# Kernel optimization log

Measured on AMD Instinct MI355X. Metric: run time of the kernel, lower is better.

Reference implementation:

```python
import jax, jax.numpy as jnp
import numpy as np

SOS = 1  # letter2index['<sos>']
EOS = 0  # letter2index['<eos>'] (embedding padding_idx)

B, T, KV, E, H, V, L = 64, 2048, 128, 256, 512, 30, 256


def _lstm_cell(x, h, c, W_ih, W_hh, b_ih, b_hh):
    # PyTorch LSTMCell: gates ordered (i, f, g, o)
    gates = x @ W_ih.T + b_ih + h @ W_hh.T + b_hh
    i, f, g, o = jnp.split(gates, 4, axis=-1)
    c_new = jax.nn.sigmoid(f) * c + jax.nn.sigmoid(i) * jnp.tanh(g)
    h_new = jax.nn.sigmoid(o) * jnp.tanh(c_new)
    return h_new, c_new


def setup_inputs() -> dict:
    root = jax.random.key(0)
    ks = jax.random.split(root, 16)

    key = jax.random.normal(ks[0], (B, T, KV), dtype=jnp.float32)
    value = jax.random.normal(ks[1], (B, T, KV), dtype=jnp.float32)
    encoder_len = jax.random.randint(ks[2], (B,), 1, T + 1)
    y = jax.random.randint(ks[3], (B, L), 0, V)

    def w(k, shape, fan_in):
        return jax.random.normal(k, shape, dtype=jnp.float32) / np.sqrt(fan_in)

    emb_weight = w(ks[4], (V, E), E).at[EOS].set(0.0)  # padding_idx row zeroed
    in1 = E + KV
    W_ih1 = w(ks[5], (4 * H, in1), in1)
    W_hh1 = w(ks[6], (4 * H, H), H)
    b_ih1 = jnp.zeros((4 * H,), jnp.float32)
    b_hh1 = jnp.zeros((4 * H,), jnp.float32)
    W_ih2 = w(ks[7], (4 * KV, H), H)
    W_hh2 = w(ks[8], (4 * KV, KV), KV)
    b_ih2 = jnp.zeros((4 * KV,), jnp.float32)
    b_hh2 = jnp.zeros((4 * KV,), jnp.float32)
    out_bias = jnp.zeros((V,), jnp.float32)

    return dict(key=key, value=value, encoder_len=encoder_len, y=y,
                emb_weight=emb_weight,
                W_ih1=W_ih1, W_hh1=W_hh1, b_ih1=b_ih1, b_hh1=b_hh1,
                W_ih2=W_ih2, W_hh2=W_hh2, b_ih2=b_ih2, b_hh2=b_hh2,
                out_bias=out_bias)


def reference(key, value, encoder_len, y, emb_weight,
              W_ih1, W_hh1, b_ih1, b_hh1,
              W_ih2, W_hh2, b_ih2, b_hh2, out_bias):
    Bq, Tq, d_k = key.shape
    mask = jnp.arange(Tq)[None, :] >= encoder_len[:, None]  # (B, T) True = padded
    scale = 1.0 / np.sqrt(d_k).astype(np.float32)

    # Teacher forcing rate 1.0 in train mode: step i uses embed(SOS) at i=0,
    # embed(y[:, i-1]) afterwards.
    ids = jnp.concatenate([jnp.full((Bq, 1), SOS, dtype=y.dtype), y[:, :-1]], axis=1)
    embeds = emb_weight[ids]               # (B, L, E)
    embeds_t = jnp.swapaxes(embeds, 0, 1)  # (L, B, E)

    h_dim = W_hh1.shape[1]
    kv_dim = W_hh2.shape[1]
    init = (jnp.zeros((Bq, h_dim), key.dtype), jnp.zeros((Bq, h_dim), key.dtype),
            jnp.zeros((Bq, kv_dim), key.dtype), jnp.zeros((Bq, kv_dim), key.dtype),
            value.mean(axis=1))  # initial context

    def step(carry, char_embed):
        h1, c1, h2, c2, context = carry
        x = jnp.concatenate([char_embed, context], axis=1)
        h1, c1 = _lstm_cell(x, h1, c1, W_ih1, W_hh1, b_ih1, b_hh1)
        h2, c2 = _lstm_cell(h1, h2, c2, W_ih2, W_hh2, b_ih2, b_hh2)
        query = h2                                             # (B, KV)
        energy = jnp.einsum('bd,btd->bt', query, key) * scale  # (B, T)
        energy = jnp.where(mask, -1e9, energy)
        attn = jax.nn.softmax(energy, axis=1)
        ctx = jnp.einsum('bt,btd->bd', attn, value)            # (B, KV)
        logits = jnp.concatenate([query, ctx], axis=1) @ emb_weight.T + out_bias
        return (h1, c1, h2, c2, ctx), (logits, attn[0])

    _, (preds, attn_plot) = jax.lax.scan(step, init, embeds_t)
    predictions = jnp.swapaxes(preds, 0, 1)  # (B, L, V)
    return predictions, attn_plot            # attn_plot: (L, T), batch element 0
```

## Files before the change

kernel.cpp:

```cpp
#include <hip/hip_runtime.h>

#define NB 256
#define NT 1024

#define BB   64
#define TTS  2048
#define DKV  128
#define EEM  256
#define HH1  512
#define VVV  30
#define LLS  256
#define SOS_ID 1
#define SCALE_F 0.088388347648318447f

#define OFF_PM    0
#define OFF_PS    256
#define OFF_PCTX  512
#define OFF_WSE   33280
#define OFF_EMBT  35328
#define OFF_H1    68096
#define OFF_C1    133632
#define OFF_H2R   166400
#define OFF_H2T   182784
#define OFF_C2    199168
#define OFF_BAR   207360
#define OFF_KBF   212992
#define OFF_VBF   8601600
#define WS_NEED_BYTES 67960832ull
#define PRED_SZ   491520

struct Params {
  const float* key; const float* value;
  const int* enc_len; const int* y;
  const float* emb;
  const float* Wih1; const float* Whh1; const float* bih1; const float* bhh1;
  const float* Wih2; const float* Whh2; const float* bih2; const float* bhh2;
  const float* obias;
  float* out; float* ws;
};

struct SMEM {
  union {
    struct {
      float ctxT[8192];
      union { float wt[8192]; float red[8192]; } u;
    } a;
    struct { float wm[16]; float wS[16]; float wctx[2048]; } c;
  };
};

__device__ __forceinline__ float sigm(float x) { return 1.f / (1.f + __expf(-x)); }
__device__ __forceinline__ float tanh_f(float x) {
  float t = __expf(-2.f * fabsf(x));
  float r = (1.f - t) / (1.f + t);
  return x < 0.f ? -r : r;
}
__device__ __forceinline__ unsigned bfr(float f) {
  unsigned u = __float_as_uint(f);
  return (u + 0x7FFFu + ((u >> 16) & 1u)) >> 16;
}
__device__ __forceinline__ float b2f(unsigned short h) {
  return __uint_as_float(((unsigned)h) << 16);
}
__device__ __forceinline__ float blo(unsigned u) { return __uint_as_float(u << 16); }
__device__ __forceinline__ float bhi(unsigned u) { return __uint_as_float(u & 0xffff0000u); }

__device__ __forceinline__ void gbar(unsigned* base, unsigned expect) {
  __syncthreads();
  if (threadIdx.x == 0) {
    __builtin_amdgcn_fence(__ATOMIC_RELEASE, "agent");
    const int grp = blockIdx.x >> 3;
    unsigned* gcnt = base + grp * 32;
    if (__hip_atomic_fetch_add(gcnt, 1u, __ATOMIC_RELAXED, __HIP_MEMORY_SCOPE_AGENT) == 7u) {
      unsigned* mcnt = base + 1024;
      if (__hip_atomic_fetch_add(mcnt, 1u, __ATOMIC_RELAXED, __HIP_MEMORY_SCOPE_AGENT) == 31u) {
        __hip_atomic_store(mcnt, 0u, __ATOMIC_RELAXED, __HIP_MEMORY_SCOPE_AGENT);
        #pragma unroll
        for (int gg = 0; gg < 32; ++gg)
          __hip_atomic_store(base + gg * 32, 0u, __ATOMIC_RELAXED, __HIP_MEMORY_SCOPE_AGENT);
        __builtin_amdgcn_fence(__ATOMIC_RELEASE, "agent");
        #pragma unroll
        for (int gg = 0; gg < 32; ++gg)
          __hip_atomic_store(base + 2048 + gg * 32, expect, __ATOMIC_RELAXED, __HIP_MEMORY_SCOPE_AGENT);
      }
    }
    unsigned* mygen = base + 2048 + grp * 32;
    int guard = 0;
    while ((int)(__hip_atomic_load(mygen, __ATOMIC_RELAXED, __HIP_MEMORY_SCOPE_AGENT) - expect) < 0) {
      __builtin_amdgcn_s_sleep(8);
      if (++guard > 10000000) break;
    }
    __builtin_amdgcn_fence(__ATOMIC_ACQUIRE, "agent");
  }
  __syncthreads();
}

__device__ __forceinline__ void mac8x4(float acc[8][4], const float* wt, int k, float4 x4) {
  float4 wa = *(const float4*)(wt + k*8);
  float4 wb = *(const float4*)(wt + k*8 + 4);
  float wr[8] = {wa.x, wa.y, wa.z, wa.w, wb.x, wb.y, wb.z, wb.w};
  float xr[4] = {x4.x, x4.y, x4.z, x4.w};
  #pragma unroll
  for (int r = 0; r < 8; ++r)
    #pragma unroll
    for (int c = 0; c < 4; ++c)
      acc[r][c] += wr[r] * xr[c];
}

__device__ __forceinline__ void gate_reduce_store(float acc[8][4], float* red, int tid) {
  #pragma unroll
  for (int r = 0; r < 8; ++r) {
    #pragma unroll
    for (int c = 0; c < 4; ++c) {
      float v = acc[r][c];
      v += __shfl_xor(v, 16);
      v += __shfl_xor(v, 32);
      acc[r][c] = v;
    }
  }
  int wv = tid >> 6, b0 = tid & 15;
  if ((tid & 63) < 16) {
    #pragma unroll
    for (int r = 0; r < 8; ++r)
      *(float4*)(red + wv*512 + r*64 + b0*4) =
        make_float4(acc[r][0], acc[r][1], acc[r][2], acc[r][3]);
  }
}

template<bool MEAN, bool BF16>
__device__ void phase_attn(const Params& p, const float* qrow,
                           const unsigned short* kbf, const unsigned short* vbf,
                           float* pm, float* pS, float* pctx, float* wsE,
                           SMEM* sm, int bj, int tid) {
  const int lane = tid & 63, w = tid >> 6;
  const int b = ((bj & 7) << 3) | ((bj >> 3) & 7);
  const int s = bj >> 6;
  const int len = MEAN ? TTS : p.enc_len[b];
  const int sub = lane & 15, grp = lane >> 4;
  const int q = 4*w + s;
  const int r0 = q*4 + grp;
  float m = -1e30f, S = 0.f;
  float ca[8] = {0.f,0.f,0.f,0.f,0.f,0.f,0.f,0.f};
  if constexpr (MEAN) {
    const float* vb = p.value + (size_t)b * TTS * DKV;
    #pragma unroll
    for (int j = 0; j < 8; ++j) {
      int t = r0 + 256*j;
      const float* vp = vb + (size_t)t * DKV + sub*8;
      float4 va = *(const float4*)vp;
      float4 vb4 = *(const float4*)(vp + 4);
      S += 1.f;
      ca[0]+=va.x;  ca[1]+=va.y;  ca[2]+=va.z;  ca[3]+=va.w;
      ca[4]+=vb4.x; ca[5]+=vb4.y; ca[6]+=vb4.z; ca[7]+=vb4.w;
    }
    m = 0.f;
  } else if (len > q*4) {
    float q8[8];
    {
      const float* qp = qrow + b*DKV + sub*8;
      float4 qa = *(const float4*)qp;
      float4 qb = *(const float4*)(qp + 4);
      q8[0]=qa.x; q8[1]=qa.y; q8[2]=qa.z; q8[3]=qa.w;
      q8[4]=qb.x; q8[5]=qb.y; q8[6]=qb.z; q8[7]=qb.w;
    }
    float e[8];
    if constexpr (BF16) {
      const unsigned short* kb  = kbf + (size_t)(b*TTS)*DKV + sub*8;
      const unsigned short* vbp = vbf + (size_t)(b*TTS)*DKV + sub*8;
      int tcs[8];
      #pragma unroll
      for (int j = 0; j < 8; ++j) {
        int t = r0 + 256*j;
        tcs[j] = t < len ? t : len - 1;
      }
      uint4 kq[8];
      #pragma unroll
      for (int j = 0; j < 8; ++j) kq[j] = *(const uint4*)(kb + (size_t)tcs[j]*DKV);
      __builtin_amdgcn_sched_barrier(0);
      #pragma unroll
      for (int j = 0; j < 8; ++j) {
        float ep = blo(kq[j].x)*q8[0] + bhi(kq[j].x)*q8[1]
                 + blo(kq[j].y)*q8[2] + bhi(kq[j].y)*q8[3]
                 + blo(kq[j].z)*q8[4] + bhi(kq[j].z)*q8[5]
                 + blo(kq[j].w)*q8[6] + bhi(kq[j].w)*q8[7];
        ep += __shfl_xor(ep, 1); ep += __shfl_xor(ep, 2);
        ep += __shfl_xor(ep, 4); ep += __shfl_xor(ep, 8);
        int t = r0 + 256*j;
        e[j] = (t < len) ? ep * SCALE_F : -1e30f;
        if (b == 0 && sub == 0 && t < len) wsE[t] = e[j];
      }
      m = fmaxf(fmaxf(fmaxf(e[0],e[1]), fmaxf(e[2],e[3])),
                fmaxf(fmaxf(e[4],e[5]), fmaxf(e[6],e[7])));
      float pr[8];
      #pragma unroll
      for (int j = 0; j < 8; ++j) {
        pr[j] = (e[j] > -1e29f) ? __expf(e[j] - m) : 0.f;
        S += pr[j];
      }
      uint4 vq[8];
      #pragma unroll
      for (int j = 0; j < 8; ++j) vq[j] = *(const uint4*)(vbp + (size_t)tcs[j]*DKV);
      __builtin_amdgcn_sched_barrier(0);
      #pragma unroll
      for (int j = 0; j < 8; ++j) {
        ca[0] += pr[j]*blo(vq[j].x); ca[1] += pr[j]*bhi(vq[j].x);
        ca[2] += pr[j]*blo(vq[j].y); ca[3] += pr[j]*bhi(vq[j].y);
        ca[4] += pr[j]*blo(vq[j].z); ca[5] += pr[j]*bhi(vq[j].z);
        ca[6] += pr[j]*blo(vq[j].w); ca[7] += pr[j]*bhi(vq[j].w);
      }
    } else {
      int tcs[8];
      #pragma unroll
      for (int j = 0; j < 8; ++j) {
        int t = r0 + 256*j;
        tcs[j] = t < len ? t : len - 1;
      }
      #pragma unroll
      for (int j = 0; j < 8; ++j) {
        const float* kp = p.key + (size_t)(b*TTS + tcs[j])*DKV + sub*8;
        float4 ka = *(const float4*)kp;
        float4 kb2 = *(const float4*)(kp + 4);
        float ep = ka.x*q8[0] + ka.y*q8[1] + ka.z*q8[2] + ka.w*q8[3]
                 + kb2.x*q8[4] + kb2.y*q8[5] + kb2.z*q8[6] + kb2.w*q8[7];
        ep += __shfl_xor(ep, 1); ep += __shfl_xor(ep, 2);
        ep += __shfl_xor(ep, 4); ep += __shfl_xor(ep, 8);
        int t = r0 + 256*j;
        e[j] = (t < len) ? ep * SCALE_F : -1e30f;
        if (b == 0 && sub == 0 && t < len) wsE[t] = e[j];
      }
      m = fmaxf(fmaxf(fmaxf(e[0],e[1]), fmaxf(e[2],e[3])),
                fmaxf(fmaxf(e[4],e[5]), fmaxf(e[6],e[7])));
      float pr[8];
      #pragma unroll
      for (int j = 0; j < 8; ++j) {
        pr[j] = (e[j] > -1e29f) ? __expf(e[j] - m) : 0.f;
        S += pr[j];
      }
      #pragma unroll
      for (int j = 0; j < 8; ++j) {
        const float* vp = p.value + (size_t)(b*TTS + tcs[j])*DKV + sub*8;
        float4 va = *(const float4*)vp;
        float4 vb4 = *(const float4*)(vp + 4);
        ca[0] += pr[j]*va.x;  ca[1] += pr[j]*va.y;
        ca[2] += pr[j]*va.z;  ca[3] += pr[j]*va.w;
        ca[4] += pr[j]*vb4.x; ca[5] += pr[j]*vb4.y;
        ca[6] += pr[j]*vb4.z; ca[7] += pr[j]*vb4.w;
      }
    }
  }
  #pragma unroll
  for (int off = 16; off <= 32; off <<= 1) {
    float mo = __shfl_xor(m, off);
    float So = __shfl_xor(S, off);
    float M2 = fmaxf(m, mo);
    float a0 = __expf(m - M2), a1 = __expf(mo - M2);
    S = S*a0 + So*a1;
    #pragma unroll
    for (int d = 0; d < 8; ++d)
      ca[d] = ca[d]*a0 + __shfl_xor(ca[d], off)*a1;
    m = M2;
  }
  if (lane == 0) { sm->c.wm[w] = m; sm->c.wS[w] = S; }
  if (grp == 0) {
    *(float4*)(sm->c.wctx + w*DKV + sub*8)     = make_float4(ca[0],ca[1],ca[2],ca[3]);
    *(float4*)(sm->c.wctx + w*DKV + sub*8 + 4) = make_float4(ca[4],ca[5],ca[6],ca[7]);
  }
  __syncthreads();
  if (tid < DKV) {
    int d = tid;
    float M = -1e30f;
    #pragma unroll
    for (int ww = 0; ww < 16; ++ww) M = fmaxf(M, sm->c.wm[ww]);
    float Z = 0.f, acc2 = 0.f;
    #pragma unroll
    for (int ww = 0; ww < 16; ++ww) {
      float aw = __expf(sm->c.wm[ww] - M);
      Z += aw * sm->c.wS[ww];
      acc2 += aw * sm->c.wctx[ww*DKV + d];
    }
    pctx[d*256 + b*4 + s] = acc2;
    if (d == 0) { pm[b*4 + s] = M; pS[b*4 + s] = Z; }
  }
}

template<bool BF16>
__global__ void __launch_bounds__(NT, 4) decoder_kernel(Params p) {
  const int tid = threadIdx.x;
  const int bj = blockIdx.x;
  float* ws = p.ws;
  unsigned* bar = (unsigned*)(ws + OFF_BAR);
  float* pm = ws + OFF_PM;
  float* pS = ws + OFF_PS;
  float* pctx = ws + OFF_PCTX;
  float* wsE = ws + OFF_WSE;
  float* embT0 = ws + OFF_EMBT;
  float* embT1 = ws + OFF_EMBT + EEM*BB;
  float* h1b0 = ws + OFF_H1;
  float* h1b1 = ws + OFF_H1 + HH1*BB;
  float* c1 = ws + OFF_C1;
  float* h2r0 = ws + OFF_H2R;
  float* h2r1 = ws + OFF_H2R + BB*DKV;
  float* h2t0 = ws + OFF_H2T;
  float* h2t1 = ws + OFF_H2T + DKV*BB;
  float* c2 = ws + OFF_C2;
  unsigned short* kbf = (unsigned short*)(ws + OFF_KBF);
  unsigned short* vbf = (unsigned short*)(ws + OFF_VBF);
  unsigned genc = 0;

  __shared__ SMEM sm;

  float wr1[8] = {0,0,0,0,0,0,0,0};
  if (tid < 896) {
    #pragma unroll
    for (int r = 0; r < 8; ++r) {
      int grow = (r >> 1)*HH1 + 2*bj + (r & 1);
      wr1[r] = (tid < 384) ? p.Wih1[(size_t)grow*384 + tid]
                           : p.Whh1[(size_t)grow*HH1 + (tid - 384)];
    }
  }
  float wr2[8] = {0,0,0,0,0,0,0,0};
  if (bj < 64 && tid < 640) {
    #pragma unroll
    for (int r = 0; r < 8; ++r) {
      int grow = (r >> 1)*DKV + 2*bj + (r & 1);
      wr2[r] = (tid < 512) ? p.Wih2[(size_t)grow*HH1 + tid]
                           : p.Whh2[(size_t)grow*DKV + (tid - 512)];
    }
  }
  float bsum1 = 0.f, bsum2 = 0.f;
  if (tid < 512) {
    int r = tid >> 6;
    int g1 = (r >> 1)*HH1 + 2*bj + (r & 1);
    bsum1 = p.bih1[g1] + p.bhh1[g1];
    if (bj < 64) {
      int g2 = (r >> 1)*DKV + 2*bj + (r & 1);
      bsum2 = p.bih2[g2] + p.bhh2[g2];
    }
  }

  {
    int gid = bj*NT + tid;
    for (int idx = gid; idx < (OFF_BAR - OFF_H1); idx += NB*NT) ws[OFF_H1 + idx] = 0.f;
    for (int idx = gid; idx < EEM*BB; idx += NB*NT) {
      int k = idx >> 6, b = idx & 63;
      embT0[k*64 + b] = p.emb[SOS_ID*EEM + k];
    }
    if constexpr (BF16) {
      const int NG = (BB*TTS*DKV) / 8;
      for (int g = gid; g < NG; g += NB*NT) {
        const float4* src = (const float4*)p.key + (size_t)g*2;
        float4 a = src[0], bq = src[1];
        uint4 o;
        o.x = bfr(a.x)  | (bfr(a.y)  << 16);
        o.y = bfr(a.z)  | (bfr(a.w)  << 16);
        o.z = bfr(bq.x) | (bfr(bq.y) << 16);
        o.w = bfr(bq.z) | (bfr(bq.w) << 16);
        ((uint4*)kbf)[g] = o;
      }
      for (int g = gid; g < NG; g += NB*NT) {
        const float4* src = (const float4*)p.value + (size_t)g*2;
        float4 a = src[0], bq = src[1];
        uint4 o;
        o.x = bfr(a.x)  | (bfr(a.y)  << 16);
        o.y = bfr(a.z)  | (bfr(a.w)  << 16);
        o.z = bfr(bq.x) | (bfr(bq.y) << 16);
        o.w = bfr(bq.z) | (bfr(bq.w) << 16);
        ((uint4*)vbf)[g] = o;
      }
    }
    phase_attn<true, BF16>(p, nullptr, kbf, vbf, pm, pS, pctx, wsE, &sm, bj, tid);
  }
  gbar(bar, ++genc);

  for (int i = 0; i <= LLS; ++i) {
    const int cur = i & 1;
    float* h1c = cur ? h1b1 : h1b0;
    const float* h1p = cur ? h1b0 : h1b1;
    float* h2rc = cur ? h2r1 : h2r0;
    const float* h2rp = cur ? h2r0 : h2r1;
    float* h2tc = cur ? h2t1 : h2t0;
    const float* h2tp = cur ? h2t0 : h2t1;
    const float* et = cur ? embT1 : embT0;
    float* etn = cur ? embT0 : embT1;

    {
      int b = tid & 63, dg = tid >> 6;
      float4 m4 = *(const float4*)(pm + b*4);
      float4 s4 = *(const float4*)(pS + b*4);
      float M = fmaxf(fmaxf(m4.x, m4.y), fmaxf(m4.z, m4.w));
      float a0 = __expf(m4.x - M), a1 = __expf(m4.y - M);
      float a2 = __expf(m4.z - M), a3 = __expf(m4.w - M);
      float Z = a0*s4.x + a1*s4.y + a2*s4.z + a3*s4.w;
      float iZ = 1.f / Z;
      a0 *= iZ; a1 *= iZ; a2 *= iZ; a3 *= iZ;
      #pragma unroll
      for (int jj = 0; jj < 8; ++jj) {
        int d = dg + jj*16;
        float4 c4 = *(const float4*)(pctx + d*256 + b*4);
        sm.a.ctxT[d*64 + b] = a0*c4.x + a1*c4.y + a2*c4.z + a3*c4.w;
      }
    }
    if (i < LLS && tid < 896) {
      *(float4*)(sm.a.u.wt + tid*8)     = make_float4(wr1[0], wr1[1], wr1[2], wr1[3]);
      *(float4*)(sm.a.u.wt + tid*8 + 4) = make_float4(wr1[4], wr1[5], wr1[6], wr1[7]);
    }
    __syncthreads();

    if (i < LLS) {
      {
        const int b0 = tid & 15, ks = tid >> 4;
        float acc[8][4];
        #pragma unroll
        for (int r = 0; r < 8; ++r) { acc[r][0]=0.f; acc[r][1]=0.f; acc[r][2]=0.f; acc[r][3]=0.f; }
        #pragma unroll
        for (int j = 0; j < 4; ++j) {
          int k = ks*4 + j;
          float4 x4 = *(const float4*)(et + k*64 + b0*4);
          mac8x4(acc, sm.a.u.wt, k, x4);
        }
        #pragma unroll
        for (int j = 0; j < 2; ++j) {
          int d = ks*2 + j;
          float4 x4 = *(const float4*)(sm.a.ctxT + d*64 + b0*4);
          mac8x4(acc, sm.a.u.wt, 256 + d, x4);
        }
        #pragma unroll
        for (int j = 0; j < 8; ++j) {
          int kk = ks*8 + j;
          float4 x4 = *(const float4*)(h1p + kk*64 + b0*4);
          mac8x4(acc, sm.a.u.wt, 384 + kk, x4);
        }
        __syncthreads();
        gate_reduce_store(acc, sm.a.u.red, tid);
      }
      __syncthreads();
      if (tid < 512) {
        int r = tid >> 6, b = tid & 63;
        float s = 0.f;
        #pragma unroll
        for (int w2 = 0; w2 < 16; ++w2) s += sm.a.u.red[w2*512 + r*64 + b];
        s += bsum1;
        sm.a.u.red[r*64 + b] = s;
      }
      __syncthreads();
      if (tid < 128) {
        int hh = tid >> 6, b = tid & 63;
        int h = 2*bj + hh;
        float gi = sm.a.u.red[(hh+0)*64 + b];
        float gf = sm.a.u.red[(hh+2)*64 + b];
        float gg = sm.a.u.red[(hh+4)*64 + b];
        float go = sm.a.u.red[(hh+6)*64 + b];
        float co = c1[h*64 + b];
        float cn = sigm(gf)*co + sigm(gi)*tanh_f(gg);
        float hn = sigm(go)*tanh_f(cn);
        c1[h*64 + b] = cn;
        h1c[h*64 + b] = hn;
      }
    }

    if (i >= 1) {
      if (tid >= 960) {
        int ln = tid - 960;
        int oi = bj*8 + (ln >> 3);
        int sub = ln & 7;
        if (oi < BB*VVV) {
          int b = oi / VVV, v = oi - b*VVV;
          float a = 0.f;
          if (sub < 4) {
            #pragma unroll 8
            for (int e0 = 0; e0 < 32; ++e0) {
              int e = sub*32 + e0;
              a += h2rp[b*DKV + e] * p.emb[v*EEM + e];
            }
          } else {
            #pragma unroll 8
            for (int e0 = 0; e0 < 32; ++e0) {
              int d = (sub - 4)*32 + e0;
              a += sm.a.ctxT[d*64 + b] * p.emb[v*EEM + 128 + d];
            }
          }
          a += __shfl_xor(a, 1); a += __shfl_xor(a, 2); a += __shfl_xor(a, 4);
          if (sub == 0) p.out[((size_t)b*LLS + (i-1))*VVV + v] = a + p.obias[v];
        }
      }
      if (tid >= 896 && tid < 904) {
        int t = bj*8 + (tid - 896);
        int len0 = p.enc_len[0];
        float v = 0.f;
        if (t < len0) {
          float m0 = pm[0], m1 = pm[1], m2 = pm[2], m3 = pm[3];
          float M = fmaxf(fmaxf(m0, m1), fmaxf(m2, m3));
          float Z = __expf(m0 - M)*pS[0] + __expf(m1 - M)*pS[1]
                  + __expf(m2 - M)*pS[2] + __expf(m3 - M)*pS[3];
          v = __expf(wsE[t] - M) / Z;
        }
        p.out[PRED_SZ + (size_t)(i-1)*TTS + t] = v;
      }
    }

    if (i == LLS) break;
    gbar(bar, ++genc);

    if (bj < 64) {
      if (tid < 640) {
        *(float4*)(sm.a.u.wt + tid*8)     = make_float4(wr2[0], wr2[1], wr2[2], wr2[3]);
        *(float4*)(sm.a.u.wt + tid*8 + 4) = make_float4(wr2[4], wr2[5], wr2[6], wr2[7]);
      }
      __syncthreads();
      {
        const int b0 = tid & 15, ks = tid >> 4;
        float acc[8][4];
        #pragma unroll
        for (int r = 0; r < 8; ++r) { acc[r][0]=0.f; acc[r][1]=0.f; acc[r][2]=0.f; acc[r][3]=0.f; }
        #pragma unroll
        for (int j = 0; j < 8; ++j) {
          int k = ks*8 + j;
          float4 x4 = *(const float4*)(h1c + k*64 + b0*4);
          mac8x4(acc, sm.a.u.wt, k, x4);
        }
        #pragma unroll
        for (int j = 0; j < 2; ++j) {
          int d = ks*2 + j;
          float4 x4 = *(const float4*)(h2tp + d*64 + b0*4);
          mac8x4(acc, sm.a.u.wt, 512 + d, x4);
        }
        __syncthreads();
        gate_reduce_store(acc, sm.a.u.red, tid);
      }
      __syncthreads();
      if (tid < 512) {
        int r = tid >> 6, b = tid & 63;
        float s = 0.f;
        #pragma unroll
        for (int w2 = 0; w2 < 16; ++w2) s += sm.a.u.red[w2*512 + r*64 + b];
        s += bsum2;
        sm.a.u.red[r*64 + b] = s;
      }
      __syncthreads();
      if (tid < 128) {
        int hh = tid >> 6, b = tid & 63;
        int d2 = 2*bj + hh;
        float gi = sm.a.u.red[(hh+0)*64 + b];
        float gf = sm.a.u.red[(hh+2)*64 + b];
        float gg = sm.a.u.red[(hh+4)*64 + b];
        float go = sm.a.u.red[(hh+6)*64 + b];
        float co = c2[d2*64 + b];
        float cn = sigm(gf)*co + sigm(gi)*tanh_f(gg);
        float hn = sigm(go)*tanh_f(cn);
        c2[d2*64 + b] = cn;
        h2rc[b*DKV + d2] = hn;
        h2tc[d2*64 + b] = hn;
      }
    } else if (bj < 128) {
      int sn = i + 1;
      if (sn < LLS && tid < 256) {
        int idx = (bj - 64)*256 + tid;
        int k = idx >> 6, b = idx & 63;
        int id = p.y[b*LLS + sn - 1];
        etn[k*64 + b] = p.emb[(size_t)id*EEM + k];
      }
    }
    gbar(bar, ++genc);

    phase_attn<false, BF16>(p, h2rc, kbf, vbf, pm, pS, pctx, wsE, &sm, bj, tid);
    gbar(bar, ++genc);
  }
}

__global__ void init_bar_kernel(unsigned* bar) {
  int i = blockIdx.x * blockDim.x + threadIdx.x;
  if (i < 4096) bar[i] = 0u;
}

extern "C" void kernel_launch(void* const* d_in, const int* in_sizes, int n_in,
                              void* d_out, int out_size, void* d_ws, size_t ws_size,
                              hipStream_t stream) {
  Params prm;
  prm.key     = (const float*)d_in[0];
  prm.value   = (const float*)d_in[1];
  prm.enc_len = (const int*)d_in[2];
  prm.y       = (const int*)d_in[3];
  prm.emb     = (const float*)d_in[4];
  prm.Wih1    = (const float*)d_in[5];
  prm.Whh1    = (const float*)d_in[6];
  prm.bih1    = (const float*)d_in[7];
  prm.bhh1    = (const float*)d_in[8];
  prm.Wih2    = (const float*)d_in[9];
  prm.Whh2    = (const float*)d_in[10];
  prm.bih2    = (const float*)d_in[11];
  prm.bhh2    = (const float*)d_in[12];
  prm.obias   = (const float*)d_in[13];
  prm.out = (float*)d_out;
  prm.ws  = (float*)d_ws;

  unsigned* bar = (unsigned*)((float*)d_ws + OFF_BAR);
  init_bar_kernel<<<16, 256, 0, stream>>>(bar);

  void* args[] = { &prm };
  if (ws_size >= WS_NEED_BYTES) {
    hipError_t e = hipLaunchCooperativeKernel((const void*)decoder_kernel<true>,
                                              dim3(NB), dim3(NT), args, 0, stream);
    if (e != hipSuccess) decoder_kernel<true><<<dim3(NB), dim3(NT), 0, stream>>>(prm);
  } else {
    hipError_t e = hipLaunchCooperativeKernel((const void*)decoder_kernel<false>,
                                              dim3(NB), dim3(NT), args, 0, stream);
    if (e != hipSuccess) decoder_kernel<false><<<dim3(NB), dim3(NT), 0, stream>>>(prm);
  }
}
```

Before: 18.51 ms.

## Prefetch attention K/V loads before grid barrier via inline asm

Splits the attention phase into an issue step and a compute step. The bf16 key/value global loads are issued with inline asm before the grid barrier, so their latency overlaps the barrier wait, and are waited on with s_waitcnt afterwards. It also remaps the block-to-batch mapping to b=bj>>2 and caches enc_len per block. The risks are that the inline asm loads bypass compiler dependency tracking and keep 64 extra VGPRs live across the barrier. The early-exit check for fully padded tiles is also dropped in the bf16 path, so those tiles now load and compute on clamped rows.

```diff
diff --git a/kernel.cpp b/kernel.cpp
--- a/kernel.cpp
+++ b/kernel.cpp
@@ -29,6 +29,8 @@
 #define WS_NEED_BYTES 67960832ull
 #define PRED_SZ   491520
 
+typedef unsigned u32x4 __attribute__((ext_vector_type(4)));
+
 struct Params {
   const float* key; const float* value;
   const int* enc_len; const int* y;
@@ -58,9 +60,6 @@
 __device__ __forceinline__ unsigned bfr(float f) {
   unsigned u = __float_as_uint(f);
   return (u + 0x7FFFu + ((u >> 16) & 1u)) >> 16;
-}
-__device__ __forceinline__ float b2f(unsigned short h) {
-  return __uint_as_float(((unsigned)h) << 16);
 }
 __device__ __forceinline__ float blo(unsigned u) { return __uint_as_float(u << 16); }
 __device__ __forceinline__ float bhi(unsigned u) { return __uint_as_float(u & 0xffff0000u); }
@@ -127,127 +126,11 @@
   }
 }
 
-template<bool MEAN, bool BF16>
-__device__ void phase_attn(const Params& p, const float* qrow,
-                           const unsigned short* kbf, const unsigned short* vbf,
-                           float* pm, float* pS, float* pctx, float* wsE,
-                           SMEM* sm, int bj, int tid) {
+__device__ __forceinline__ void attn_merge_tail(float m, float S, float ca[8],
+                                                float* pm, float* pS, float* pctx,
+                                                SMEM* sm, int b, int s, int tid) {
   const int lane = tid & 63, w = tid >> 6;
-  const int b = ((bj & 7) << 3) | ((bj >> 3) & 7);
-  const int s = bj >> 6;
-  const int len = MEAN ? TTS : p.enc_len[b];
   const int sub = lane & 15, grp = lane >> 4;
-  const int q = 4*w + s;
-  const int r0 = q*4 + grp;
-  float m = -1e30f, S = 0.f;
-  float ca[8] = {0.f,0.f,0.f,0.f,0.f,0.f,0.f,0.f};
-  if constexpr (MEAN) {
-    const float* vb = p.value + (size_t)b * TTS * DKV;
-    #pragma unroll
-    for (int j = 0; j < 8; ++j) {
-      int t = r0 + 256*j;
-      const float* vp = vb + (size_t)t * DKV + sub*8;
-      float4 va = *(const float4*)vp;
-      float4 vb4 = *(const float4*)(vp + 4);
-      S += 1.f;
-      ca[0]+=va.x;  ca[1]+=va.y;  ca[2]+=va.z;  ca[3]+=va.w;
-      ca[4]+=vb4.x; ca[5]+=vb4.y; ca[6]+=vb4.z; ca[7]+=vb4.w;
-    }
-    m = 0.f;
-  } else if (len > q*4) {
-    float q8[8];
-    {
-      const float* qp = qrow + b*DKV + sub*8;
-      float4 qa = *(const float4*)qp;
-      float4 qb = *(const float4*)(qp + 4);
-      q8[0]=qa.x; q8[1]=qa.y; q8[2]=qa.z; q8[3]=qa.w;
-      q8[4]=qb.x; q8[5]=qb.y; q8[6]=qb.z; q8[7]=qb.w;
-    }
-    float e[8];
-    if constexpr (BF16) {
-      const unsigned short* kb  = kbf + (size_t)(b*TTS)*DKV + sub*8;
-      const unsigned short* vbp = vbf + (size_t)(b*TTS)*DKV + sub*8;
-      int tcs[8];
-      #pragma unroll
-      for (int j = 0; j < 8; ++j) {
-        int t = r0 + 256*j;
-        tcs[j] = t < len ? t : len - 1;
-      }
-      uint4 kq[8];
-      #pragma unroll
-      for (int j = 0; j < 8; ++j) kq[j] = *(const uint4*)(kb + (size_t)tcs[j]*DKV);
-      __builtin_amdgcn_sched_barrier(0);
-      #pragma unroll
-      for (int j = 0; j < 8; ++j) {
-        float ep = blo(kq[j].x)*q8[0] + bhi(kq[j].x)*q8[1]
-                 + blo(kq[j].y)*q8[2] + bhi(kq[j].y)*q8[3]
-                 + blo(kq[j].z)*q8[4] + bhi(kq[j].z)*q8[5]
-                 + blo(kq[j].w)*q8[6] + bhi(kq[j].w)*q8[7];
-        ep += __shfl_xor(ep, 1); ep += __shfl_xor(ep, 2);
-        ep += __shfl_xor(ep, 4); ep += __shfl_xor(ep, 8);
-        int t = r0 + 256*j;
-        e[j] = (t < len) ? ep * SCALE_F : -1e30f;
-        if (b == 0 && sub == 0 && t < len) wsE[t] = e[j];
-      }
-      m = fmaxf(fmaxf(fmaxf(e[0],e[1]), fmaxf(e[2],e[3])),
-                fmaxf(fmaxf(e[4],e[5]), fmaxf(e[6],e[7])));
-      float pr[8];
-      #pragma unroll
-      for (int j = 0; j < 8; ++j) {
-        pr[j] = (e[j] > -1e29f) ? __expf(e[j] - m) : 0.f;
-        S += pr[j];
-      }
-      uint4 vq[8];
-      #pragma unroll
-      for (int j = 0; j < 8; ++j) vq[j] = *(const uint4*)(vbp + (size_t)tcs[j]*DKV);
-      __builtin_amdgcn_sched_barrier(0);
-      #pragma unroll
-      for (int j = 0; j < 8; ++j) {
-        ca[0] += pr[j]*blo(vq[j].x); ca[1] += pr[j]*bhi(vq[j].x);
-        ca[2] += pr[j]*blo(vq[j].y); ca[3] += pr[j]*bhi(vq[j].y);
-        ca[4] += pr[j]*blo(vq[j].z); ca[5] += pr[j]*bhi(vq[j].z);
-        ca[6] += pr[j]*blo(vq[j].w); ca[7] += pr[j]*bhi(vq[j].w);
-      }
-    } else {
-      int tcs[8];
-      #pragma unroll
-      for (int j = 0; j < 8; ++j) {
-        int t = r0 + 256*j;
-        tcs[j] = t < len ? t : len - 1;
-      }
-      #pragma unroll
-      for (int j = 0; j < 8; ++j) {
-        const float* kp = p.key + (size_t)(b*TTS + tcs[j])*DKV + sub*8;
-        float4 ka = *(const float4*)kp;
-        float4 kb2 = *(const float4*)(kp + 4);
-        float ep = ka.x*q8[0] + ka.y*q8[1] + ka.z*q8[2] + ka.w*q8[3]
-                 + kb2.x*q8[4] + kb2.y*q8[5] + kb2.z*q8[6] + kb2.w*q8[7];
-        ep += __shfl_xor(ep, 1); ep += __shfl_xor(ep, 2);
-        ep += __shfl_xor(ep, 4); ep += __shfl_xor(ep, 8);
-        int t = r0 + 256*j;
-        e[j] = (t < len) ? ep * SCALE_F : -1e30f;
-        if (b == 0 && sub == 0 && t < len) wsE[t] = e[j];
-      }
-      m = fmaxf(fmaxf(fmaxf(e[0],e[1]), fmaxf(e[2],e[3])),
-                fmaxf(fmaxf(e[4],e[5]), fmaxf(e[6],e[7])));
-      float pr[8];
-      #pragma unroll
-      for (int j = 0; j < 8; ++j) {
-        pr[j] = (e[j] > -1e29f) ? __expf(e[j] - m) : 0.f;
-        S += pr[j];
-      }
-      #pragma unroll
-      for (int j = 0; j < 8; ++j) {
-        const float* vp = p.value + (size_t)(b*TTS + tcs[j])*DKV + sub*8;
-        float4 va = *(const float4*)vp;
-        float4 vb4 = *(const float4*)(vp + 4);
-        ca[0] += pr[j]*va.x;  ca[1] += pr[j]*va.y;
-        ca[2] += pr[j]*va.z;  ca[3] += pr[j]*va.w;
-        ca[4] += pr[j]*vb4.x; ca[5] += pr[j]*vb4.y;
-        ca[6] += pr[j]*vb4.z; ca[7] += pr[j]*vb4.w;
-      }
-    }
-  }
   #pragma unroll
   for (int off = 16; off <= 32; off <<= 1) {
     float mo = __shfl_xor(m, off);
@@ -281,6 +164,147 @@
     pctx[d*256 + b*4 + s] = acc2;
     if (d == 0) { pm[b*4 + s] = M; pS[b*4 + s] = Z; }
   }
+}
+
+__device__ void attn_mean(const Params& p, float* pm, float* pS, float* pctx,
+                          SMEM* sm, int bj, int tid) {
+  const int lane = tid & 63, w = tid >> 6;
+  const int b = bj >> 2, s = bj & 3;
+  const int sub = lane & 15, grp = lane >> 4;
+  const int q = 4*w + s;
+  const int r0 = q*4 + grp;
+  float S = 0.f;
+  float ca[8] = {0.f,0.f,0.f,0.f,0.f,0.f,0.f,0.f};
+  const float* vb = p.value + (size_t)b * TTS * DKV;
+  #pragma unroll
+  for (int j = 0; j < 8; ++j) {
+    int t = r0 + 256*j;
+    const float* vp = vb + (size_t)t * DKV + sub*8;
+    float4 va = *(const float4*)vp;
+    float4 vb4 = *(const float4*)(vp + 4);
+    S += 1.f;
+    ca[0]+=va.x;  ca[1]+=va.y;  ca[2]+=va.z;  ca[3]+=va.w;
+    ca[4]+=vb4.x; ca[5]+=vb4.y; ca[6]+=vb4.z; ca[7]+=vb4.w;
+  }
+  attn_merge_tail(0.f, S, ca, pm, pS, pctx, sm, b, s, tid);
+}
+
+__device__ __forceinline__ void attn_issue(const unsigned short* kbf,
+                                           const unsigned short* vbf,
+                                           int b, int s, int len, int tid,
+                                           u32x4 (&kq)[8], u32x4 (&vq)[8]) {
+  const int lane = tid & 63, w = tid >> 6;
+  const int sub = lane & 15, grp = lane >> 4;
+  const int q = 4*w + s;
+  const int r0 = q*4 + grp;
+  unsigned voff[8];
+  #pragma unroll
+  for (int j = 0; j < 8; ++j) {
+    int t = r0 + 256*j;
+    int tc = t < len ? t : len - 1;
+    voff[j] = (unsigned)((b*TTS + tc)*DKV + sub*8) * 2u;
+  }
+  #pragma unroll
+  for (int j = 0; j < 8; ++j)
+    asm volatile("global_load_dwordx4 %0, %1, %2"
+                 : "=v"(kq[j]) : "v"(voff[j]), "s"(kbf));
+  #pragma unroll
+  for (int j = 0; j < 8; ++j)
+    asm volatile("global_load_dwordx4 %0, %1, %2"
+                 : "=v"(vq[j]) : "v"(voff[j]), "s"(vbf));
+}
+
+template<bool BF16>
+__device__ void attn_compute(const Params& p, const float* qrow,
+                             u32x4 (&kq)[8], u32x4 (&vq)[8],
+                             float* pm, float* pS, float* pctx, float* wsE,
+                             SMEM* sm, int b, int s, int len, int tid) {
+  const int lane = tid & 63, w = tid >> 6;
+  const int sub = lane & 15, grp = lane >> 4;
+  const int q = 4*w + s;
+  const int r0 = q*4 + grp;
+  float m = -1e30f, S = 0.f;
+  float ca[8] = {0.f,0.f,0.f,0.f,0.f,0.f,0.f,0.f};
+  float q8[8];
+  {
+    const float* qp = qrow + b*DKV + sub*8;
+    float4 qa = *(const float4*)qp;
+    float4 qb = *(const float4*)(qp + 4);
+    q8[0]=qa.x; q8[1]=qa.y; q8[2]=qa.z; q8[3]=qa.w;
+    q8[4]=qb.x; q8[5]=qb.y; q8[6]=qb.z; q8[7]=qb.w;
+  }
+  if constexpr (BF16) {
+    asm volatile("s_waitcnt vmcnt(0)" ::: "memory");
+    __builtin_amdgcn_sched_barrier(0);
+    float e[8];
+    #pragma unroll
+    for (int j = 0; j < 8; ++j) {
+      float ep = blo(kq[j][0])*q8[0] + bhi(kq[j][0])*q8[1]
+               + blo(kq[j][1])*q8[2] + bhi(kq[j][1])*q8[3]
+               + blo(kq[j][2])*q8[4] + bhi(kq[j][2])*q8[5]
+               + blo(kq[j][3])*q8[6] + bhi(kq[j][3])*q8[7];
+      ep += __shfl_xor(ep, 1); ep += __shfl_xor(ep, 2);
+      ep += __shfl_xor(ep, 4); ep += __shfl_xor(ep, 8);
+      int t = r0 + 256*j;
+      e[j] = (t < len) ? ep * SCALE_F : -1e30f;
+      if (b == 0 && sub == 0 && t < len) wsE[t] = e[j];
+    }
+    m = fmaxf(fmaxf(fmaxf(e[0],e[1]), fmaxf(e[2],e[3])),
+              fmaxf(fmaxf(e[4],e[5]), fmaxf(e[6],e[7])));
+    float pr[8];
+    #pragma unroll
+    for (int j = 0; j < 8; ++j) {
+      pr[j] = (e[j] > -1e29f) ? __expf(e[j] - m) : 0.f;
+      S += pr[j];
+    }
+    #pragma unroll
+    for (int j = 0; j < 8; ++j) {
+      ca[0] += pr[j]*blo(vq[j][0]); ca[1] += pr[j]*bhi(vq[j][0]);
+      ca[2] += pr[j]*blo(vq[j][1]); ca[3] += pr[j]*bhi(vq[j][1]);
+      ca[4] += pr[j]*blo(vq[j][2]); ca[5] += pr[j]*bhi(vq[j][2]);
+      ca[6] += pr[j]*blo(vq[j][3]); ca[7] += pr[j]*bhi(vq[j][3]);
+    }
+  } else if (len > q*4) {
+    int tcs[8];
+    #pragma unroll
+    for (int j = 0; j < 8; ++j) {
+      int t = r0 + 256*j;
+      tcs[j] = t < len ? t : len - 1;
+    }
+    float e[8];
+    #pragma unroll
+    for (int j = 0; j < 8; ++j) {
+      const float* kp = p.key + (size_t)(b*TTS + tcs[j])*DKV + sub*8;
+      float4 ka = *(const float4*)kp;
+      float4 kb2 = *(const float4*)(kp + 4);
+      float ep = ka.x*q8[0] + ka.y*q8[1] + ka.z*q8[2] + ka.w*q8[3]
+               + kb2.x*q8[4] + kb2.y*q8[5] + kb2.z*q8[6] + kb2.w*q8[7];
+      ep += __shfl_xor(ep, 1); ep += __shfl_xor(ep, 2);
+      ep += __shfl_xor(ep, 4); ep += __shfl_xor(ep, 8);
+      int t = r0 + 256*j;
+      e[j] = (t < len) ? ep * SCALE_F : -1e30f;
+      if (b == 0 && sub == 0 && t < len) wsE[t] = e[j];
+    }
+    m = fmaxf(fmaxf(fmaxf(e[0],e[1]), fmaxf(e[2],e[3])),
+              fmaxf(fmaxf(e[4],e[5]), fmaxf(e[6],e[7])));
+    float pr[8];
+    #pragma unroll
+    for (int j = 0; j < 8; ++j) {
+      pr[j] = (e[j] > -1e29f) ? __expf(e[j] - m) : 0.f;
+      S += pr[j];
+    }
+    #pragma unroll
+    for (int j = 0; j < 8; ++j) {
+      const float* vp = p.value + (size_t)(b*TTS + tcs[j])*DKV + sub*8;
+      float4 va = *(const float4*)vp;
+      float4 vb4 = *(const float4*)(vp + 4);
+      ca[0] += pr[j]*va.x;  ca[1] += pr[j]*va.y;
+      ca[2] += pr[j]*va.z;  ca[3] += pr[j]*va.w;
+      ca[4] += pr[j]*vb4.x; ca[5] += pr[j]*vb4.y;
+      ca[6] += pr[j]*vb4.z; ca[7] += pr[j]*vb4.w;
+    }
+  }
+  attn_merge_tail(m, S, ca, pm, pS, pctx, sm, b, s, tid);
 }
 
 template<bool BF16>
@@ -307,6 +331,9 @@
   unsigned short* vbf = (unsigned short*)(ws + OFF_VBF);
   unsigned genc = 0;
 
+  const int b_my = bj >> 2, s_my = bj & 3;
+  const int len_my = p.enc_len[b_my];
+
   __shared__ SMEM sm;
 
   float wr1[8] = {0,0,0,0,0,0,0,0};
@@ -368,9 +395,11 @@
         ((uint4*)vbf)[g] = o;
       }
     }
-    phase_attn<true, BF16>(p, nullptr, kbf, vbf, pm, pS, pctx, wsE, &sm, bj, tid);
+    attn_mean(p, pm, pS, pctx, &sm, bj, tid);
   }
   gbar(bar, ++genc);
+
+  u32x4 kq[8], vq[8];
 
   for (int i = 0; i <= LLS; ++i) {
     const int cur = i & 1;
@@ -560,9 +589,11 @@
         etn[k*64 + b] = p.emb[(size_t)id*EEM + k];
       }
     }
+
+    if constexpr (BF16) attn_issue(kbf, vbf, b_my, s_my, len_my, tid, kq, vq);
     gbar(bar, ++genc);
 
-    phase_attn<false, BF16>(p, h2rc, kbf, vbf, pm, pS, pctx, wsE, &sm, bj, tid);
+    attn_compute<BF16>(p, h2rc, kq, vq, pm, pS, pctx, wsE, &sm, b_my, s_my, len_my, tid);
     gbar(bar, ++genc);
   }
 }
```

Result: faster. 17.73 ms (-4.2%).

## Balance attention work across blocks by per-batch encoder length

Applied to the files above, without the earlier changes.

Replaces the fixed 4-blocks-per-batch attention split with a length-proportional assignment of the 256 blocks to batch rows, so rows with long encoder sequences get more blocks and short ones fewer. Each block then processes up to 8 timesteps per thread at a stride set by its row's block count, and the context merge loops over a variable number of partials. It also issues the V loads alongside the K loads to overlap memory latency. The cost is extra per-block setup work, variable-length merge loops, and higher register pressure from holding K and V at once.

```diff
diff --git a/kernel.cpp b/kernel.cpp
--- a/kernel.cpp
+++ b/kernel.cpp
@@ -59,9 +59,6 @@
   unsigned u = __float_as_uint(f);
   return (u + 0x7FFFu + ((u >> 16) & 1u)) >> 16;
 }
-__device__ __forceinline__ float b2f(unsigned short h) {
-  return __uint_as_float(((unsigned)h) << 16);
-}
 __device__ __forceinline__ float blo(unsigned u) { return __uint_as_float(u << 16); }
 __device__ __forceinline__ float bhi(unsigned u) { return __uint_as_float(u & 0xffff0000u); }
 
@@ -127,34 +124,81 @@
   }
 }
 
-template<bool MEAN, bool BF16>
-__device__ void phase_attn(const Params& p, const float* qrow,
-                           const unsigned short* kbf, const unsigned short* vbf,
-                           float* pm, float* pS, float* pctx, float* wsE,
-                           SMEM* sm, int bj, int tid) {
+__device__ __forceinline__ void attn_merge_tail(float m, float S, float ca[8],
+                                                float* pm, float* pS, float* pctx,
+                                                SMEM* sm, int sidx, int tid) {
   const int lane = tid & 63, w = tid >> 6;
-  const int b = ((bj & 7) << 3) | ((bj >> 3) & 7);
-  const int s = bj >> 6;
-  const int len = MEAN ? TTS : p.enc_len[b];
   const int sub = lane & 15, grp = lane >> 4;
-  const int q = 4*w + s;
-  const int r0 = q*4 + grp;
+  #pragma unroll
+  for (int off = 16; off <= 32; off <<= 1) {
+    float mo = __shfl_xor(m, off);
+    float So = __shfl_xor(S, off);
+    float M2 = fmaxf(m, mo);
+    float a0 = __expf(m - M2), a1 = __expf(mo - M2);
+    S = S*a0 + So*a1;
+    #pragma unroll
+    for (int d = 0; d < 8; ++d)
+      ca[d] = ca[d]*a0 + __shfl_xor(ca[d], off)*a1;
+    m = M2;
+  }
+  if (lane == 0) { sm->c.wm[w] = m; sm->c.wS[w] = S; }
+  if (grp == 0) {
+    *(float4*)(sm->c.wctx + w*DKV + sub*8)     = make_float4(ca[0],ca[1],ca[2],ca[3]);
+    *(float4*)(sm->c.wctx + w*DKV + sub*8 + 4) = make_float4(ca[4],ca[5],ca[6],ca[7]);
+  }
+  __syncthreads();
+  if (tid < DKV) {
+    int d = tid;
+    float M = -1e30f;
+    #pragma unroll
+    for (int ww = 0; ww < 16; ++ww) M = fmaxf(M, sm->c.wm[ww]);
+    float Z = 0.f, acc2 = 0.f;
+    #pragma unroll
+    for (int ww = 0; ww < 16; ++ww) {
+      float aw = __expf(sm->c.wm[ww] - M);
+      Z += aw * sm->c.wS[ww];
+      acc2 += aw * sm->c.wctx[ww*DKV + d];
+    }
+    pctx[d*256 + sidx] = acc2;
+    if (d == 0) { pm[sidx] = M; pS[sidx] = Z; }
+  }
+}
+
+__device__ void attn_mean(const Params& p, float* pm, float* pS, float* pctx,
+                          SMEM* sm, int b, int is, int ns, int bj, int tid) {
+  const int lane = tid & 63, w = tid >> 6;
+  const int sub = lane & 15, grp = lane >> 4;
+  const int Q = is*16 + w;
+  const int stride = 64*ns;
+  const int r0 = Q*4 + grp;
+  float S = 0.f;
+  float ca[8] = {0.f,0.f,0.f,0.f,0.f,0.f,0.f,0.f};
+  const float* vb = p.value + (size_t)b * TTS * DKV;
+  for (int t = r0; t < TTS; t += stride) {
+    const float* vp = vb + (size_t)t * DKV + sub*8;
+    float4 va = *(const float4*)vp;
+    float4 vb4 = *(const float4*)(vp + 4);
+    S += 1.f;
+    ca[0]+=va.x;  ca[1]+=va.y;  ca[2]+=va.z;  ca[3]+=va.w;
+    ca[4]+=vb4.x; ca[5]+=vb4.y; ca[6]+=vb4.z; ca[7]+=vb4.w;
+  }
+  attn_merge_tail(0.f, S, ca, pm, pS, pctx, sm, bj, tid);
+}
+
+template<bool BF16>
+__device__ void phase_attn_main(const Params& p, const float* qrow,
+                                const unsigned short* kbf, const unsigned short* vbf,
+                                float* pm, float* pS, float* pctx, float* wsE,
+                                SMEM* sm, int b, int is, int ns, int len,
+                                int bj, int tid) {
+  const int lane = tid & 63, w = tid >> 6;
+  const int sub = lane & 15, grp = lane >> 4;
+  const int Q = is*16 + w;
+  const int stride = 64*ns;
+  const int r0 = Q*4 + grp;
   float m = -1e30f, S = 0.f;
   float ca[8] = {0.f,0.f,0.f,0.f,0.f,0.f,0.f,0.f};
-  if constexpr (MEAN) {
-    const float* vb = p.value + (size_t)b * TTS * DKV;
-    #pragma unroll
-    for (int j = 0; j < 8; ++j) {
-      int t = r0 + 256*j;
-      const float* vp = vb + (size_t)t * DKV + sub*8;
-      float4 va = *(const float4*)vp;
-      float4 vb4 = *(const float4*)(vp + 4);
-      S += 1.f;
-      ca[0]+=va.x;  ca[1]+=va.y;  ca[2]+=va.z;  ca[3]+=va.w;
-      ca[4]+=vb4.x; ca[5]+=vb4.y; ca[6]+=vb4.z; ca[7]+=vb4.w;
-    }
-    m = 0.f;
-  } else if (len > q*4) {
+  if (len > Q*4) {
     float q8[8];
     {
       const float* qp = qrow + b*DKV + sub*8;
@@ -163,19 +207,21 @@
       q8[0]=qa.x; q8[1]=qa.y; q8[2]=qa.z; q8[3]=qa.w;
       q8[4]=qb.x; q8[5]=qb.y; q8[6]=qb.z; q8[7]=qb.w;
     }
+    int tcs[8];
+    #pragma unroll
+    for (int j = 0; j < 8; ++j) {
+      int t = r0 + stride*j;
+      tcs[j] = t < len ? t : len - 1;
+    }
     float e[8];
     if constexpr (BF16) {
       const unsigned short* kb  = kbf + (size_t)(b*TTS)*DKV + sub*8;
       const unsigned short* vbp = vbf + (size_t)(b*TTS)*DKV + sub*8;
-      int tcs[8];
-      #pragma unroll
-      for (int j = 0; j < 8; ++j) {
-        int t = r0 + 256*j;
-        tcs[j] = t < len ? t : len - 1;
-      }
-      uint4 kq[8];
-      #pragma unroll
-      for (int j = 0; j < 8; ++j) kq[j] = *(const uint4*)(kb + (size_t)tcs[j]*DKV);
+      uint4 kq[8], vq[8];
+      #pragma unroll
+      for (int j = 0; j < 8; ++j) kq[j] = *(const uint4*)(kb  + (size_t)tcs[j]*DKV);
+      #pragma unroll
+      for (int j = 0; j < 8; ++j) vq[j] = *(const uint4*)(vbp + (size_t)tcs[j]*DKV);
       __builtin_amdgcn_sched_barrier(0);
       #pragma unroll
       for (int j = 0; j < 8; ++j) {
@@ -185,7 +231,7 @@
                  + blo(kq[j].w)*q8[6] + bhi(kq[j].w)*q8[7];
         ep += __shfl_xor(ep, 1); ep += __shfl_xor(ep, 2);
         ep += __shfl_xor(ep, 4); ep += __shfl_xor(ep, 8);
-        int t = r0 + 256*j;
+        int t = r0 + stride*j;
         e[j] = (t < len) ? ep * SCALE_F : -1e30f;
         if (b == 0 && sub == 0 && t < len) wsE[t] = e[j];
       }
@@ -197,10 +243,6 @@
         pr[j] = (e[j] > -1e29f) ? __expf(e[j] - m) : 0.f;
         S += pr[j];
       }
-      uint4 vq[8];
-      #pragma unroll
-      for (int j = 0; j < 8; ++j) vq[j] = *(const uint4*)(vbp + (size_t)tcs[j]*DKV);
-      __builtin_amdgcn_sched_barrier(0);
       #pragma unroll
       for (int j = 0; j < 8; ++j) {
         ca[0] += pr[j]*blo(vq[j].x); ca[1] += pr[j]*bhi(vq[j].x);
@@ -209,12 +251,6 @@
         ca[6] += pr[j]*blo(vq[j].w); ca[7] += pr[j]*bhi(vq[j].w);
       }
     } else {
-      int tcs[8];
-      #pragma unroll
-      for (int j = 0; j < 8; ++j) {
-        int t = r0 + 256*j;
-        tcs[j] = t < len ? t : len - 1;
-      }
       #pragma unroll
       for (int j = 0; j < 8; ++j) {
         const float* kp = p.key + (size_t)(b*TTS + tcs[j])*DKV + sub*8;
@@ -224,7 +260,7 @@
                  + kb2.x*q8[4] + kb2.y*q8[5] + kb2.z*q8[6] + kb2.w*q8[7];
         ep += __shfl_xor(ep, 1); ep += __shfl_xor(ep, 2);
         ep += __shfl_xor(ep, 4); ep += __shfl_xor(ep, 8);
-        int t = r0 + 256*j;
+        int t = r0 + stride*j;
         e[j] = (t < len) ? ep * SCALE_F : -1e30f;
         if (b == 0 && sub == 0 && t < len) wsE[t] = e[j];
       }
@@ -248,39 +284,7 @@
       }
     }
   }
-  #pragma unroll
-  for (int off = 16; off <= 32; off <<= 1) {
-    float mo = __shfl_xor(m, off);
-    float So = __shfl_xor(S, off);
-    float M2 = fmaxf(m, mo);
-    float a0 = __expf(m - M2), a1 = __expf(mo - M2);
-    S = S*a0 + So*a1;
-    #pragma unroll
-    for (int d = 0; d < 8; ++d)
-      ca[d] = ca[d]*a0 + __shfl_xor(ca[d], off)*a1;
-    m = M2;
-  }
-  if (lane == 0) { sm->c.wm[w] = m; sm->c.wS[w] = S; }
-  if (grp == 0) {
-    *(float4*)(sm->c.wctx + w*DKV + sub*8)     = make_float4(ca[0],ca[1],ca[2],ca[3]);
-    *(float4*)(sm->c.wctx + w*DKV + sub*8 + 4) = make_float4(ca[4],ca[5],ca[6],ca[7]);
-  }
-  __syncthreads();
-  if (tid < DKV) {
-    int d = tid;
-    float M = -1e30f;
-    #pragma unroll
-    for (int ww = 0; ww < 16; ++ww) M = fmaxf(M, sm->c.wm[ww]);
-    float Z = 0.f, acc2 = 0.f;
-    #pragma unroll
-    for (int ww = 0; ww < 16; ++ww) {
-      float aw = __expf(sm->c.wm[ww] - M);
-      Z += aw * sm->c.wS[ww];
-      acc2 += aw * sm->c.wctx[ww*DKV + d];
-    }
-    pctx[d*256 + b*4 + s] = acc2;
-    if (d == 0) { pm[b*4 + s] = M; pS[b*4 + s] = Z; }
-  }
+  attn_merge_tail(m, S, ca, pm, pS, pctx, sm, bj, tid);
 }
 
 template<bool BF16>
@@ -308,6 +312,57 @@
   unsigned genc = 0;
 
   __shared__ SMEM sm;
+  __shared__ int s_lenv[64];
+  __shared__ int s_ns[64];
+  __shared__ int s_base[64];
+  __shared__ int s_binfo[4];
+
+  if (tid < 64) s_lenv[tid] = p.enc_len[tid];
+  __syncthreads();
+  if (tid == 0) {
+    int R = 0;
+    for (int b = 0; b < 64; ++b) R += s_lenv[b];
+    int tot = 0;
+    for (int b = 0; b < 64; ++b) {
+      int need = (s_lenv[b] + 511) >> 9;
+      if (need < 1) need = 1;
+      int v = (int)((256LL * s_lenv[b]) / R);
+      if (v < need) v = need;
+      s_ns[b] = v; tot += v;
+    }
+    while (tot < 256) {
+      int bb = 0; float best = -1.f;
+      for (int b = 0; b < 64; ++b) {
+        float r = (float)s_lenv[b] / (float)s_ns[b];
+        if (r > best) { best = r; bb = b; }
+      }
+      s_ns[bb]++; tot++;
+    }
+    while (tot > 256) {
+      int bb = -1; float best = 1e30f;
+      for (int b = 0; b < 64; ++b) {
+        int need = (s_lenv[b] + 511) >> 9;
+        if (need < 1) need = 1;
+        if (s_ns[b] > need) {
+          float r = (float)s_lenv[b] / (float)s_ns[b];
+          if (r < best) { best = r; bb = b; }
+        }
+      }
+      if (bb < 0) break;
+      s_ns[bb]--; tot--;
+    }
+    int acc = 0;
+    for (int b = 0; b < 64; ++b) { s_base[b] = acc; acc += s_ns[b]; }
+    for (int b = 0; b < 64; ++b) {
+      if (bj >= s_base[b] && bj < s_base[b] + s_ns[b]) {
+        s_binfo[0] = b; s_binfo[1] = bj - s_base[b];
+        s_binfo[2] = s_ns[b]; s_binfo[3] = s_lenv[b];
+      }
+    }
+  }
+  __syncthreads();
+  const int b_my = s_binfo[0], is_my = s_binfo[1];
+  const int ns_my = s_binfo[2], len_my = s_binfo[3];
 
   float wr1[8] = {0,0,0,0,0,0,0,0};
   if (tid < 896) {
@@ -368,7 +423,7 @@
         ((uint4*)vbf)[g] = o;
       }
     }
-    phase_attn<true, BF16>(p, nullptr, kbf, vbf, pm, pS, pctx, wsE, &sm, bj, tid);
+    attn_mean(p, pm, pS, pctx, &sm, b_my, is_my, ns_my, bj, tid);
   }
   gbar(bar, ++genc);
 
@@ -385,20 +440,23 @@
 
     {
       int b = tid & 63, dg = tid >> 6;
-      float4 m4 = *(const float4*)(pm + b*4);
-      float4 s4 = *(const float4*)(pS + b*4);
-      float M = fmaxf(fmaxf(m4.x, m4.y), fmaxf(m4.z, m4.w));
-      float a0 = __expf(m4.x - M), a1 = __expf(m4.y - M);
-      float a2 = __expf(m4.z - M), a3 = __expf(m4.w - M);
-      float Z = a0*s4.x + a1*s4.y + a2*s4.z + a3*s4.w;
+      int nsb = s_ns[b], bas = s_base[b];
+      float M = -1e30f;
+      for (int k = 0; k < nsb; ++k) M = fmaxf(M, pm[bas + k]);
+      float Z = 0.f;
+      float accv[8] = {0.f,0.f,0.f,0.f,0.f,0.f,0.f,0.f};
+      for (int k = 0; k < nsb; ++k) {
+        int idx = bas + k;
+        float aw = __expf(pm[idx] - M);
+        Z += aw * pS[idx];
+        #pragma unroll
+        for (int jj = 0; jj < 8; ++jj)
+          accv[jj] += aw * pctx[(dg + jj*16)*256 + idx];
+      }
       float iZ = 1.f / Z;
-      a0 *= iZ; a1 *= iZ; a2 *= iZ; a3 *= iZ;
-      #pragma unroll
-      for (int jj = 0; jj < 8; ++jj) {
-        int d = dg + jj*16;
-        float4 c4 = *(const float4*)(pctx + d*256 + b*4);
-        sm.a.ctxT[d*64 + b] = a0*c4.x + a1*c4.y + a2*c4.z + a3*c4.w;
-      }
+      #pragma unroll
+      for (int jj = 0; jj < 8; ++jj)
+        sm.a.ctxT[(dg + jj*16)*64 + b] = accv[jj] * iZ;
     }
     if (i < LLS && tid < 896) {
       *(float4*)(sm.a.u.wt + tid*8)     = make_float4(wr1[0], wr1[1], wr1[2], wr1[3]);
@@ -485,13 +543,14 @@
       }
       if (tid >= 896 && tid < 904) {
         int t = bj*8 + (tid - 896);
-        int len0 = p.enc_len[0];
+        int len0 = s_lenv[0];
         float v = 0.f;
         if (t < len0) {
-          float m0 = pm[0], m1 = pm[1], m2 = pm[2], m3 = pm[3];
-          float M = fmaxf(fmaxf(m0, m1), fmaxf(m2, m3));
-          float Z = __expf(m0 - M)*pS[0] + __expf(m1 - M)*pS[1]
-                  + __expf(m2 - M)*pS[2] + __expf(m3 - M)*pS[3];
+          int n0 = s_ns[0];
+          float M = -1e30f;
+          for (int k = 0; k < n0; ++k) M = fmaxf(M, pm[k]);
+          float Z = 0.f;
+          for (int k = 0; k < n0; ++k) Z += __expf(pm[k] - M) * pS[k];
           v = __expf(wsE[t] - M) / Z;
         }
         p.out[PRED_SZ + (size_t)(i-1)*TTS + t] = v;
@@ -562,7 +621,8 @@
     }
     gbar(bar, ++genc);
 
-    phase_attn<false, BF16>(p, h2rc, kbf, vbf, pm, pS, pctx, wsE, &sm, bj, tid);
+    phase_attn_main<BF16>(p, h2rc, kbf, vbf, pm, pS, pctx, wsE, &sm,
+                          b_my, is_my, ns_my, len_my, bj, tid);
     gbar(bar, ++genc);
   }
 }
```

New measurement: 19.80 ms. +7.0%, slower.
